# Optimization experiments

Measured on AMD Instinct MI355X. Metric: run time of the kernel, lower is better.

## Reference

```python
import jax, jax.numpy as jnp
import numpy as np

N_NODES = 50000
N_EDGES = 800000


def _glorot(key, shape):
    fan_in, fan_out = shape
    lim = float(np.sqrt(6.0 / (fan_in + fan_out)))
    return jax.random.uniform(key, shape, jnp.float32, -lim, lim)


def setup_inputs() -> dict:
    key = jax.random.key(0)
    ks = jax.random.split(key, 8)
    x = jax.random.normal(ks[0], (N_NODES, 2), jnp.float32)
    edge_index = jax.random.randint(ks[1], (2, N_EDGES), 0, N_NODES, jnp.int64)
    edge_weight = jax.random.uniform(ks[2], (N_EDGES,), jnp.float32)
    return {
        "x": x,
        "edge_index": edge_index,
        "edge_weight": edge_weight,
        "W1": _glorot(ks[3], (2, 128)),
        "b1": jnp.zeros((128,), jnp.float32),
        "W2": _glorot(ks[4], (128, 64)),
        "b2": jnp.zeros((64,), jnp.float32),
        "W3": _glorot(ks[5], (64, 1)),
        "b3": jnp.zeros((1,), jnp.float32),
    }


def _gcn_conv(x, W, b, src, dst, ew, n_nodes):
    # PyG GCNConv with normalize=False: out[i] = sum_{e:(j->i)} ew[e] * (x_j @ W) + b
    h = x @ W                       # [N, F_out] tiny GEMM
    msg = h[src] * ew[:, None]      # [E, F_out] gather + scale
    out = jax.ops.segment_sum(msg, dst, num_segments=n_nodes)  # scatter-add
    return out + b


def reference(x, edge_index, edge_weight, W1, b1, W2, b2, W3, b3):
    src, dst = edge_index[0], edge_index[1]  # source_to_target flow: aggregate at dst
    n = x.shape[0]
    h1 = jax.nn.relu(_gcn_conv(x, W1, b1, src, dst, edge_weight, n))
    # dropout is a no-op in eval mode
    h2 = jax.nn.relu(_gcn_conv(h1, W2, b2, src, dst, edge_weight, n))
    h3 = _gcn_conv(h2, W3, b3, src, dst, edge_weight, n)  # [N, 1]
    return h3.squeeze(-1)  # [N]
```

## Files before the change

### kernel.cpp

```cpp
#include <hip/hip_runtime.h>
#include <hip/hip_fp16.h>

#define N_NODES 50000
#define N_EDGES 800000
#define BSHIFT 7
#define NBKT 391
#define CAP 3072
#define TILE 2048
#define BIN_THREADS 512
#define SL_THREADS 512

typedef _Float16 f16x8 __attribute__((ext_vector_type(8)));
typedef float f32x4 __attribute__((ext_vector_type(4)));
typedef float f32x2 __attribute__((ext_vector_type(2)));

__device__ __forceinline__ float edge_w(unsigned p) {
    return __half2float(__ushort_as_half((unsigned short)(p >> 16)));
}

__device__ __forceinline__ unsigned char f32_to_fp8(float v) {
    int w = __builtin_amdgcn_cvt_pk_fp8_f32(v, v, 0, false);
    return (unsigned char)(w & 0xFF);
}

__global__ __launch_bounds__(BIN_THREADS) void bin_edges(
    const int* __restrict__ src, const int* __restrict__ dstA,
    const float* __restrict__ ew, int* __restrict__ bcur,
    uint2* __restrict__ brec) {
    __shared__ unsigned pk[TILE];
    __shared__ unsigned short sdst[TILE];
    __shared__ uint2 rec[TILE];
    __shared__ int cnt[NBKT];
    __shared__ int lofs[NBKT];
    __shared__ int cbase[NBKT];
    __shared__ int wsum[8];
    __shared__ int wpre[8];

    int t = threadIdx.x;
    int lane = t & 63, wid = t >> 6;
    int e0 = blockIdx.x * TILE;
    int nmax = N_EDGES - e0;
    if (nmax > TILE) nmax = TILE;
    if (nmax < 0) nmax = 0;
    if (t < NBKT) cnt[t] = 0;
    __syncthreads();
    for (int i = t; i < nmax; i += BIN_THREADS) {
        int e = e0 + i;
        int d = dstA[e];
        unsigned hw = (unsigned)__half_as_ushort(__float2half(ew[e]));
        pk[i] = (unsigned)src[e] | (hw << 16);
        sdst[i] = (unsigned short)d;
        atomicAdd(&cnt[d >> BSHIFT], 1);
    }
    __syncthreads();
    int v = (t < NBKT) ? cnt[t] : 0;
    int s = v;
#pragma unroll
    for (int off = 1; off < 64; off <<= 1) {
        int u = __shfl_up(s, off);
        if (lane >= off) s += u;
    }
    if (lane == 63) wsum[wid] = s;
    __syncthreads();
    if (t < 8) {
        int a = 0;
        for (int i = 0; i < t; i++) a += wsum[i];
        wpre[t] = a;
    }
    __syncthreads();
    int incl = s + wpre[wid];
    if (t < NBKT) {
        lofs[t] = incl - v;
        cbase[t] = t * CAP + (v ? atomicAdd(&bcur[t], v) : 0);
        cnt[t] = 0;
    }
    __syncthreads();
    for (int i = t; i < nmax; i += BIN_THREADS) {
        int d = sdst[i];
        int bk = d >> BSHIFT;
        int pos = lofs[bk] + atomicAdd(&cnt[bk], 1);
        rec[pos] = make_uint2(pk[i], (unsigned)d);
    }
    __syncthreads();
    for (int i = t; i < nmax; i += BIN_THREADS) {
        uint2 r = rec[i];
        int bk = (int)(r.y >> BSHIFT);
        int g = cbase[bk] + (i - lofs[bk]);
        brec[g] = r;
    }
}

__global__ __launch_bounds__(SL_THREADS) void sort_l1(
    const int* __restrict__ bcur, const uint2* __restrict__ brec,
    const float* __restrict__ x,
    const float* __restrict__ W1, const float* __restrict__ b1,
    const float* __restrict__ W2,
    unsigned* __restrict__ sorted, int2* __restrict__ rowspan,
    unsigned char* __restrict__ t2) {
    __shared__ unsigned spk[CAP];
    __shared__ int nh[128], lcur[128];
    __shared__ float nodeA[128], nodeB[128];
    __shared__ __align__(16) __half w2t[64][136];
    __shared__ __align__(16) float w1r0[128];
    __shared__ __align__(16) float w1r1[128];
    __shared__ __align__(16) float b1s[128];
    __shared__ int wsum2[2];

    int b = blockIdx.x;
    int t = threadIdx.x;
    int lane = t & 63, wid = t >> 6;
    int base = b * CAP;
    int n = bcur[b];
    if (n > CAP) n = CAP;

    for (int idx = t; idx < 128 * 64; idx += SL_THREADS) {
        int k = idx >> 6, nn = idx & 63;
        w2t[nn][k] = __float2half(W2[idx]);
    }
    if (t < 128) {
        w1r0[t] = W1[t];
        w1r1[t] = W1[128 + t];
        b1s[t]  = b1[t];
        nh[t] = 0;
        lcur[t] = 0;
        nodeA[t] = 0.f;
        nodeB[t] = 0.f;
    }
    __syncthreads();

    unsigned rp[6];
    int rd[6];
#pragma unroll
    for (int i = 0; i < 6; i++) {
        int e = t + i * SL_THREADS;
        if (e < n) {
            uint2 r = brec[base + e];
            rp[i] = r.x;
            rd[i] = (int)(r.y & 127u);
            atomicAdd(&nh[rd[i]], 1);
            float w = edge_w(r.x);
            float2 xv = ((const float2*)x)[r.x & 0xFFFF];
            atomicAdd(&nodeA[rd[i]], w * xv.x);
            atomicAdd(&nodeB[rd[i]], w * xv.y);
        }
    }
    __syncthreads();

    int v = (t < 128) ? nh[t] : 0;
    int s = v;
#pragma unroll
    for (int off = 1; off < 64; off <<= 1) {
        int u = __shfl_up(s, off);
        if (lane >= off) s += u;
    }
    if (lane == 63 && wid < 2) wsum2[wid] = s;
    __syncthreads();
    if (t < 128) {
        int incl = s + (wid ? wsum2[0] : 0);
        int ex = incl - v;
        int node = (b << BSHIFT) + t;
        if (node < N_NODES) rowspan[node] = make_int2(base + ex, base + ex + v);
        nh[t] = ex;
    }
    __syncthreads();

#pragma unroll
    for (int i = 0; i < 6; i++) {
        int e = t + i * SL_THREADS;
        if (e < n) {
            int pos = nh[rd[i]] + atomicAdd(&lcur[rd[i]], 1);
            spk[pos] = rp[i];
        }
    }
    __syncthreads();
    for (int e = t; e < n; e += SL_THREADS) sorted[base + e] = spk[e];

    int wave = t >> 6;
    int m0 = wave * 16;
    int fr = lane & 15;
    int kb = (lane >> 4) * 8;
    float a0 = nodeA[m0 + fr];
    float a1 = nodeB[m0 + fr];
    f32x4 acc0 = {0.f, 0.f, 0.f, 0.f};
    f32x4 acc1 = {0.f, 0.f, 0.f, 0.f};
    f32x4 acc2 = {0.f, 0.f, 0.f, 0.f};
    f32x4 acc3 = {0.f, 0.f, 0.f, 0.f};
#pragma unroll
    for (int k0 = 0; k0 < 128; k0 += 32) {
        f16x8 av;
#pragma unroll
        for (int j = 0; j < 8; j++) {
            int k = k0 + kb + j;
            float h = fmaxf(fmaf(a0, w1r0[k], fmaf(a1, w1r1[k], b1s[k])), 0.f);
            av[j] = (_Float16)h;
        }
        f16x8 bv0 = *(const f16x8*)&w2t[ 0 + fr][k0 + kb];
        f16x8 bv1 = *(const f16x8*)&w2t[16 + fr][k0 + kb];
        f16x8 bv2 = *(const f16x8*)&w2t[32 + fr][k0 + kb];
        f16x8 bv3 = *(const f16x8*)&w2t[48 + fr][k0 + kb];
        acc0 = __builtin_amdgcn_mfma_f32_16x16x32_f16(av, bv0, acc0, 0, 0, 0);
        acc1 = __builtin_amdgcn_mfma_f32_16x16x32_f16(av, bv1, acc1, 0, 0, 0);
        acc2 = __builtin_amdgcn_mfma_f32_16x16x32_f16(av, bv2, acc2, 0, 0, 0);
        acc3 = __builtin_amdgcn_mfma_f32_16x16x32_f16(av, bv3, acc3, 0, 0, 0);
    }
    int rowb = (b << BSHIFT) + m0 + ((lane >> 4) & 3) * 4;
#pragma unroll
    for (int r = 0; r < 4; r++) {
        int node = rowb + r;
        if (node < N_NODES) {
            unsigned char* o = t2 + node * 64 + fr;
            o[0]  = f32_to_fp8(acc0[r]);
            o[16] = f32_to_fp8(acc1[r]);
            o[32] = f32_to_fp8(acc2[r]);
            o[48] = f32_to_fp8(acc3[r]);
        }
    }
}

__global__ void gather2_dot3(const int2* __restrict__ rowspan, const unsigned* __restrict__ sorted,
                             const unsigned char* __restrict__ t2, const float* __restrict__ b2,
                             const float* __restrict__ W3, float* __restrict__ t3) {
    int gtid = blockIdx.x * blockDim.x + threadIdx.x;
    int node = gtid >> 6;
    int lane = threadIdx.x & 63;
    if (node >= N_NODES) return;
    int eg  = lane >> 3;
    int fli = lane & 7;
    int2 sp = rowspan[node];
    float a0 = 0.f, a1 = 0.f, a2 = 0.f, a3 = 0.f, a4 = 0.f, a5 = 0.f, a6 = 0.f, a7 = 0.f;
    int e = sp.x + eg;
    for (; e + 8 < sp.y; e += 16) {
        unsigned p0 = sorted[e];
        unsigned p1 = sorted[e + 8];
        uint2 q0 = *(const uint2*)(t2 + (p0 & 0xFFFF) * 64 + fli * 8);
        uint2 q1 = *(const uint2*)(t2 + (p1 & 0xFFFF) * 64 + fli * 8);
        float w0 = edge_w(p0), w1 = edge_w(p1);
        f32x2 f;
        f = __builtin_amdgcn_cvt_pk_f32_fp8(q0.x, false); a0 = fmaf(w0, f.x, a0); a1 = fmaf(w0, f.y, a1);
        f = __builtin_amdgcn_cvt_pk_f32_fp8(q0.x, true);  a2 = fmaf(w0, f.x, a2); a3 = fmaf(w0, f.y, a3);
        f = __builtin_amdgcn_cvt_pk_f32_fp8(q0.y, false); a4 = fmaf(w0, f.x, a4); a5 = fmaf(w0, f.y, a5);
        f = __builtin_amdgcn_cvt_pk_f32_fp8(q0.y, true);  a6 = fmaf(w0, f.x, a6); a7 = fmaf(w0, f.y, a7);
        f = __builtin_amdgcn_cvt_pk_f32_fp8(q1.x, false); a0 = fmaf(w1, f.x, a0); a1 = fmaf(w1, f.y, a1);
        f = __builtin_amdgcn_cvt_pk_f32_fp8(q1.x, true);  a2 = fmaf(w1, f.x, a2); a3 = fmaf(w1, f.y, a3);
        f = __builtin_amdgcn_cvt_pk_f32_fp8(q1.y, false); a4 = fmaf(w1, f.x, a4); a5 = fmaf(w1, f.y, a5);
        f = __builtin_amdgcn_cvt_pk_f32_fp8(q1.y, true);  a6 = fmaf(w1, f.x, a6); a7 = fmaf(w1, f.y, a7);
    }
    if (e < sp.y) {
        unsigned p = sorted[e];
        uint2 q = *(const uint2*)(t2 + (p & 0xFFFF) * 64 + fli * 8);
        float w = edge_w(p);
        f32x2 f;
        f = __builtin_amdgcn_cvt_pk_f32_fp8(q.x, false); a0 = fmaf(w, f.x, a0); a1 = fmaf(w, f.y, a1);
        f = __builtin_amdgcn_cvt_pk_f32_fp8(q.x, true);  a2 = fmaf(w, f.x, a2); a3 = fmaf(w, f.y, a3);
        f = __builtin_amdgcn_cvt_pk_f32_fp8(q.y, false); a4 = fmaf(w, f.x, a4); a5 = fmaf(w, f.y, a5);
        f = __builtin_amdgcn_cvt_pk_f32_fp8(q.y, true);  a6 = fmaf(w, f.x, a6); a7 = fmaf(w, f.y, a7);
    }
#pragma unroll
    for (int off = 8; off < 64; off <<= 1) {
        a0 += __shfl_xor(a0, off); a1 += __shfl_xor(a1, off);
        a2 += __shfl_xor(a2, off); a3 += __shfl_xor(a3, off);
        a4 += __shfl_xor(a4, off); a5 += __shfl_xor(a5, off);
        a6 += __shfl_xor(a6, off); a7 += __shfl_xor(a7, off);
    }
    float4 bA = *(const float4*)(b2 + fli * 8);
    float4 bB = *(const float4*)(b2 + fli * 8 + 4);
    float4 wA = *(const float4*)(W3 + fli * 8);
    float4 wB = *(const float4*)(W3 + fli * 8 + 4);
    float h = fmaxf(a0 + bA.x, 0.f) * wA.x + fmaxf(a1 + bA.y, 0.f) * wA.y +
              fmaxf(a2 + bA.z, 0.f) * wA.z + fmaxf(a3 + bA.w, 0.f) * wA.w +
              fmaxf(a4 + bB.x, 0.f) * wB.x + fmaxf(a5 + bB.y, 0.f) * wB.y +
              fmaxf(a6 + bB.z, 0.f) * wB.z + fmaxf(a7 + bB.w, 0.f) * wB.w;
#pragma unroll
    for (int off = 1; off < 8; off <<= 1) h += __shfl_xor(h, off);
    if (lane == 0) t3[node] = h;
}

__global__ void gather3(const int2* __restrict__ rowspan, const unsigned* __restrict__ sorted,
                        const float* __restrict__ t3, const float* __restrict__ b3,
                        float* __restrict__ out) {
    int gtid = blockIdx.x * blockDim.x + threadIdx.x;
    int wid = gtid >> 6;
    int lane = threadIdx.x & 63;
    int sub = lane >> 3;
    int sl  = lane & 7;
    int node = wid * 8 + sub;
    if (node >= N_NODES) return;
    int2 sp = rowspan[node];
    float acc = 0.f;
    for (int e = sp.x + sl; e < sp.y; e += 8) {
        unsigned p = sorted[e];
        acc = fmaf(edge_w(p), t3[p & 0xFFFF], acc);
    }
#pragma unroll
    for (int off = 1; off < 8; off <<= 1) acc += __shfl_xor(acc, off);
    if (sl == 0) out[node] = acc + b3[0];
}

extern "C" void kernel_launch(void* const* d_in, const int* in_sizes, int n_in,
                              void* d_out, int out_size, void* d_ws, size_t ws_size,
                              hipStream_t stream) {
    const float* x  = (const float*)d_in[0];
    const int*   ei = (const int*)d_in[1];
    const float* ew = (const float*)d_in[2];
    const float* W1 = (const float*)d_in[3];
    const float* b1 = (const float*)d_in[4];
    const float* W2 = (const float*)d_in[5];
    const float* b2 = (const float*)d_in[6];
    const float* W3 = (const float*)d_in[7];
    const float* b3 = (const float*)d_in[8];
    float* out = (float*)d_out;

    const int* src = ei;
    const int* dst = ei + N_EDGES;

    char* p = (char*)d_ws;
    int*  bcur    = (int*)p;            p += NBKT * sizeof(int);
    p = (char*)(((uintptr_t)p + 15) & ~(uintptr_t)15);
    int2* rowspan = (int2*)p;           p += N_NODES * sizeof(int2);
    uint2* brec   = (uint2*)p;          p += (long)NBKT * CAP * sizeof(uint2);
    unsigned* sorted = (unsigned*)p;    p += (long)NBKT * CAP * sizeof(unsigned);
    unsigned char* t2 = (unsigned char*)p; p += 64L * N_NODES;
    float* t3     = (float*)p;          p += N_NODES * sizeof(float);

    hipMemsetAsync(bcur, 0, NBKT * sizeof(int), stream);

    bin_edges<<<NBKT, BIN_THREADS, 0, stream>>>(src, dst, ew, bcur, brec);

    sort_l1<<<NBKT, SL_THREADS, 0, stream>>>(bcur, brec, x, W1, b1, W2, sorted, rowspan, t2);

    gather2_dot3<<<(N_NODES * 64 + 255) / 256, 256, 0, stream>>>(rowspan, sorted, t2, b2, W3, t3);

    gather3<<<((N_NODES + 7) / 8 * 64 + 255) / 256, 256, 0, stream>>>(rowspan, sorted, t3, b3, out);
}
```

Before: 136.8 us.

## Replace CSR sort and per-node gathers with bucket-local LDS atomic aggregation

Removes the per-bucket counting sort, rowspan and sorted-edge arrays. Layers 2 and 3 now stream the unsorted bucket records and accumulate into shared-memory per-node accumulators with LDS float atomics. Layer 2 is split across two blocks per bucket, each handling half of the features, and the two partial dot products are combined with global atomics into t3, which is zeroed by an enlarged memset. This drops a sort pass and the sorted-array traffic, in exchange for many LDS atomics (8 per edge-subgroup) and nondeterministic float summation order.

```diff
diff --git a/kernel.cpp b/kernel.cpp
--- a/kernel.cpp
+++ b/kernel.cpp
@@ -8,7 +8,7 @@
 #define CAP 3072
 #define TILE 2048
 #define BIN_THREADS 512
-#define SL_THREADS 512
+#define THREADS 512
 
 typedef _Float16 f16x8 __attribute__((ext_vector_type(8)));
 typedef float f32x4 __attribute__((ext_vector_type(4)));
@@ -90,30 +90,24 @@
     }
 }
 
-__global__ __launch_bounds__(SL_THREADS) void sort_l1(
+__global__ __launch_bounds__(THREADS) void l1_mfma(
     const int* __restrict__ bcur, const uint2* __restrict__ brec,
     const float* __restrict__ x,
     const float* __restrict__ W1, const float* __restrict__ b1,
-    const float* __restrict__ W2,
-    unsigned* __restrict__ sorted, int2* __restrict__ rowspan,
-    unsigned char* __restrict__ t2) {
-    __shared__ unsigned spk[CAP];
-    __shared__ int nh[128], lcur[128];
-    __shared__ float nodeA[128], nodeB[128];
+    const float* __restrict__ W2, unsigned char* __restrict__ t2) {
     __shared__ __align__(16) __half w2t[64][136];
     __shared__ __align__(16) float w1r0[128];
     __shared__ __align__(16) float w1r1[128];
     __shared__ __align__(16) float b1s[128];
-    __shared__ int wsum2[2];
+    __shared__ float nodeA[128], nodeB[128];
 
     int b = blockIdx.x;
     int t = threadIdx.x;
-    int lane = t & 63, wid = t >> 6;
     int base = b * CAP;
     int n = bcur[b];
     if (n > CAP) n = CAP;
 
-    for (int idx = t; idx < 128 * 64; idx += SL_THREADS) {
+    for (int idx = t; idx < 128 * 64; idx += THREADS) {
         int k = idx >> 6, nn = idx & 63;
         w2t[nn][k] = __float2half(W2[idx]);
     }
@@ -121,61 +115,22 @@
         w1r0[t] = W1[t];
         w1r1[t] = W1[128 + t];
         b1s[t]  = b1[t];
-        nh[t] = 0;
-        lcur[t] = 0;
         nodeA[t] = 0.f;
         nodeB[t] = 0.f;
     }
     __syncthreads();
 
-    unsigned rp[6];
-    int rd[6];
-#pragma unroll
-    for (int i = 0; i < 6; i++) {
-        int e = t + i * SL_THREADS;
-        if (e < n) {
-            uint2 r = brec[base + e];
-            rp[i] = r.x;
-            rd[i] = (int)(r.y & 127u);
-            atomicAdd(&nh[rd[i]], 1);
-            float w = edge_w(r.x);
-            float2 xv = ((const float2*)x)[r.x & 0xFFFF];
-            atomicAdd(&nodeA[rd[i]], w * xv.x);
-            atomicAdd(&nodeB[rd[i]], w * xv.y);
-        }
-    }
-    __syncthreads();
-
-    int v = (t < 128) ? nh[t] : 0;
-    int s = v;
-#pragma unroll
-    for (int off = 1; off < 64; off <<= 1) {
-        int u = __shfl_up(s, off);
-        if (lane >= off) s += u;
-    }
-    if (lane == 63 && wid < 2) wsum2[wid] = s;
-    __syncthreads();
-    if (t < 128) {
-        int incl = s + (wid ? wsum2[0] : 0);
-        int ex = incl - v;
-        int node = (b << BSHIFT) + t;
-        if (node < N_NODES) rowspan[node] = make_int2(base + ex, base + ex + v);
-        nh[t] = ex;
-    }
-    __syncthreads();
-
-#pragma unroll
-    for (int i = 0; i < 6; i++) {
-        int e = t + i * SL_THREADS;
-        if (e < n) {
-            int pos = nh[rd[i]] + atomicAdd(&lcur[rd[i]], 1);
-            spk[pos] = rp[i];
-        }
-    }
-    __syncthreads();
-    for (int e = t; e < n; e += SL_THREADS) sorted[base + e] = spk[e];
-
-    int wave = t >> 6;
+    for (int e = t; e < n; e += THREADS) {
+        uint2 r = brec[base + e];
+        float w = edge_w(r.x);
+        float2 xv = ((const float2*)x)[r.x & 0xFFFF];
+        int dlow = (int)(r.y & 127u);
+        atomicAdd(&nodeA[dlow], w * xv.x);
+        atomicAdd(&nodeB[dlow], w * xv.y);
+    }
+    __syncthreads();
+
+    int wave = t >> 6, lane = t & 63;
     int m0 = wave * 16;
     int fr = lane & 15;
     int kb = (lane >> 4) * 8;
@@ -203,7 +158,7 @@
         acc2 = __builtin_amdgcn_mfma_f32_16x16x32_f16(av, bv2, acc2, 0, 0, 0);
         acc3 = __builtin_amdgcn_mfma_f32_16x16x32_f16(av, bv3, acc3, 0, 0, 0);
     }
-    int rowb = (b << BSHIFT) + m0 + ((lane >> 4) & 3) * 4;
+    int rowb = (b << BSHIFT) + m0 + (lane >> 4) * 4;
 #pragma unroll
     for (int r = 0; r < 4; r++) {
         int node = rowb + r;
@@ -217,83 +172,75 @@
     }
 }
 
-__global__ void gather2_dot3(const int2* __restrict__ rowspan, const unsigned* __restrict__ sorted,
-                             const unsigned char* __restrict__ t2, const float* __restrict__ b2,
-                             const float* __restrict__ W3, float* __restrict__ t3) {
-    int gtid = blockIdx.x * blockDim.x + threadIdx.x;
-    int node = gtid >> 6;
-    int lane = threadIdx.x & 63;
-    if (node >= N_NODES) return;
-    int eg  = lane >> 3;
-    int fli = lane & 7;
-    int2 sp = rowspan[node];
-    float a0 = 0.f, a1 = 0.f, a2 = 0.f, a3 = 0.f, a4 = 0.f, a5 = 0.f, a6 = 0.f, a7 = 0.f;
-    int e = sp.x + eg;
-    for (; e + 8 < sp.y; e += 16) {
-        unsigned p0 = sorted[e];
-        unsigned p1 = sorted[e + 8];
-        uint2 q0 = *(const uint2*)(t2 + (p0 & 0xFFFF) * 64 + fli * 8);
-        uint2 q1 = *(const uint2*)(t2 + (p1 & 0xFFFF) * 64 + fli * 8);
-        float w0 = edge_w(p0), w1 = edge_w(p1);
+__global__ __launch_bounds__(THREADS) void l2_dot(
+    const int* __restrict__ bcur, const uint2* __restrict__ brec,
+    const unsigned char* __restrict__ t2, const float* __restrict__ b2,
+    const float* __restrict__ W3, float* __restrict__ t3) {
+    __shared__ float hacc[128][36];
+    __shared__ float b2s[32], w3s[32];
+    int bb = blockIdx.x;
+    int b = bb >> 1, half = bb & 1;
+    int t = threadIdx.x;
+    int base = b * CAP;
+    int n = bcur[b];
+    if (n > CAP) n = CAP;
+
+    for (int i = t; i < 128 * 36; i += THREADS) ((float*)hacc)[i] = 0.f;
+    if (t < 32) { b2s[t] = b2[half * 32 + t]; w3s[t] = W3[half * 32 + t]; }
+    __syncthreads();
+
+    int total = n * 4;
+    for (int s = t; s < total; s += THREADS) {
+        int e = s >> 2, sub = s & 3;
+        uint2 r = brec[base + e];
+        float w = edge_w(r.x);
+        int dlow = (int)(r.y & 127u);
+        uint2 q = *(const uint2*)(t2 + (r.x & 0xFFFF) * 64 + half * 32 + sub * 8);
+        float* hrow = &hacc[dlow][sub * 8];
         f32x2 f;
-        f = __builtin_amdgcn_cvt_pk_f32_fp8(q0.x, false); a0 = fmaf(w0, f.x, a0); a1 = fmaf(w0, f.y, a1);
-        f = __builtin_amdgcn_cvt_pk_f32_fp8(q0.x, true);  a2 = fmaf(w0, f.x, a2); a3 = fmaf(w0, f.y, a3);
-        f = __builtin_amdgcn_cvt_pk_f32_fp8(q0.y, false); a4 = fmaf(w0, f.x, a4); a5 = fmaf(w0, f.y, a5);
-        f = __builtin_amdgcn_cvt_pk_f32_fp8(q0.y, true);  a6 = fmaf(w0, f.x, a6); a7 = fmaf(w0, f.y, a7);
-        f = __builtin_amdgcn_cvt_pk_f32_fp8(q1.x, false); a0 = fmaf(w1, f.x, a0); a1 = fmaf(w1, f.y, a1);
-        f = __builtin_amdgcn_cvt_pk_f32_fp8(q1.x, true);  a2 = fmaf(w1, f.x, a2); a3 = fmaf(w1, f.y, a3);
-        f = __builtin_amdgcn_cvt_pk_f32_fp8(q1.y, false); a4 = fmaf(w1, f.x, a4); a5 = fmaf(w1, f.y, a5);
-        f = __builtin_amdgcn_cvt_pk_f32_fp8(q1.y, true);  a6 = fmaf(w1, f.x, a6); a7 = fmaf(w1, f.y, a7);
-    }
-    if (e < sp.y) {
-        unsigned p = sorted[e];
-        uint2 q = *(const uint2*)(t2 + (p & 0xFFFF) * 64 + fli * 8);
-        float w = edge_w(p);
-        f32x2 f;
-        f = __builtin_amdgcn_cvt_pk_f32_fp8(q.x, false); a0 = fmaf(w, f.x, a0); a1 = fmaf(w, f.y, a1);
-        f = __builtin_amdgcn_cvt_pk_f32_fp8(q.x, true);  a2 = fmaf(w, f.x, a2); a3 = fmaf(w, f.y, a3);
-        f = __builtin_amdgcn_cvt_pk_f32_fp8(q.y, false); a4 = fmaf(w, f.x, a4); a5 = fmaf(w, f.y, a5);
-        f = __builtin_amdgcn_cvt_pk_f32_fp8(q.y, true);  a6 = fmaf(w, f.x, a6); a7 = fmaf(w, f.y, a7);
-    }
-#pragma unroll
-    for (int off = 8; off < 64; off <<= 1) {
-        a0 += __shfl_xor(a0, off); a1 += __shfl_xor(a1, off);
-        a2 += __shfl_xor(a2, off); a3 += __shfl_xor(a3, off);
-        a4 += __shfl_xor(a4, off); a5 += __shfl_xor(a5, off);
-        a6 += __shfl_xor(a6, off); a7 += __shfl_xor(a7, off);
-    }
-    float4 bA = *(const float4*)(b2 + fli * 8);
-    float4 bB = *(const float4*)(b2 + fli * 8 + 4);
-    float4 wA = *(const float4*)(W3 + fli * 8);
-    float4 wB = *(const float4*)(W3 + fli * 8 + 4);
-    float h = fmaxf(a0 + bA.x, 0.f) * wA.x + fmaxf(a1 + bA.y, 0.f) * wA.y +
-              fmaxf(a2 + bA.z, 0.f) * wA.z + fmaxf(a3 + bA.w, 0.f) * wA.w +
-              fmaxf(a4 + bB.x, 0.f) * wB.x + fmaxf(a5 + bB.y, 0.f) * wB.y +
-              fmaxf(a6 + bB.z, 0.f) * wB.z + fmaxf(a7 + bB.w, 0.f) * wB.w;
-#pragma unroll
-    for (int off = 1; off < 8; off <<= 1) h += __shfl_xor(h, off);
-    if (lane == 0) t3[node] = h;
-}
-
-__global__ void gather3(const int2* __restrict__ rowspan, const unsigned* __restrict__ sorted,
-                        const float* __restrict__ t3, const float* __restrict__ b3,
-                        float* __restrict__ out) {
-    int gtid = blockIdx.x * blockDim.x + threadIdx.x;
-    int wid = gtid >> 6;
-    int lane = threadIdx.x & 63;
-    int sub = lane >> 3;
-    int sl  = lane & 7;
-    int node = wid * 8 + sub;
-    if (node >= N_NODES) return;
-    int2 sp = rowspan[node];
+        f = __builtin_amdgcn_cvt_pk_f32_fp8(q.x, false);
+        atomicAdd(&hrow[0], w * f.x); atomicAdd(&hrow[1], w * f.y);
+        f = __builtin_amdgcn_cvt_pk_f32_fp8(q.x, true);
+        atomicAdd(&hrow[2], w * f.x); atomicAdd(&hrow[3], w * f.y);
+        f = __builtin_amdgcn_cvt_pk_f32_fp8(q.y, false);
+        atomicAdd(&hrow[4], w * f.x); atomicAdd(&hrow[5], w * f.y);
+        f = __builtin_amdgcn_cvt_pk_f32_fp8(q.y, true);
+        atomicAdd(&hrow[6], w * f.x); atomicAdd(&hrow[7], w * f.y);
+    }
+    __syncthreads();
+
+    int nodeL = t >> 2, q4 = t & 3;
     float acc = 0.f;
-    for (int e = sp.x + sl; e < sp.y; e += 8) {
-        unsigned p = sorted[e];
-        acc = fmaf(edge_w(p), t3[p & 0xFFFF], acc);
-    }
-#pragma unroll
-    for (int off = 1; off < 8; off <<= 1) acc += __shfl_xor(acc, off);
-    if (sl == 0) out[node] = acc + b3[0];
+#pragma unroll
+    for (int j = 0; j < 8; j++) {
+        int d = q4 * 8 + j;
+        acc += fmaxf(hacc[nodeL][d] + b2s[d], 0.f) * w3s[d];
+    }
+    acc += __shfl_xor(acc, 1);
+    acc += __shfl_xor(acc, 2);
+    int node = (b << BSHIFT) + nodeL;
+    if (q4 == 0 && node < N_NODES) atomicAdd(&t3[node], acc);
+}
+
+__global__ __launch_bounds__(THREADS) void l3_out(
+    const int* __restrict__ bcur, const uint2* __restrict__ brec,
+    const float* __restrict__ t3, const float* __restrict__ b3,
+    float* __restrict__ out) {
+    __shared__ float nacc[128];
+    int b = blockIdx.x;
+    int t = threadIdx.x;
+    int base = b * CAP;
+    int n = bcur[b];
+    if (n > CAP) n = CAP;
+    if (t < 128) nacc[t] = 0.f;
+    __syncthreads();
+    for (int e = t; e < n; e += THREADS) {
+        uint2 r = brec[base + e];
+        atomicAdd(&nacc[r.y & 127u], edge_w(r.x) * t3[r.x & 0xFFFF]);
+    }
+    __syncthreads();
+    int node = (b << BSHIFT) + t;
+    if (t < 128 && node < N_NODES) out[node] = nacc[t] + b3[0];
 }
 
 extern "C" void kernel_launch(void* const* d_in, const int* in_sizes, int n_in,
@@ -314,21 +261,21 @@
     const int* dst = ei + N_EDGES;
 
     char* p = (char*)d_ws;
-    int*  bcur    = (int*)p;            p += NBKT * sizeof(int);
+    int*  bcur = (int*)p;               p += NBKT * sizeof(int);
     p = (char*)(((uintptr_t)p + 15) & ~(uintptr_t)15);
-    int2* rowspan = (int2*)p;           p += N_NODES * sizeof(int2);
-    uint2* brec   = (uint2*)p;          p += (long)NBKT * CAP * sizeof(uint2);
-    unsigned* sorted = (unsigned*)p;    p += (long)NBKT * CAP * sizeof(unsigned);
+    float* t3  = (float*)p;             p += N_NODES * sizeof(float);
+    size_t zbytes = (size_t)(p - (char*)d_ws);
+    p = (char*)(((uintptr_t)p + 15) & ~(uintptr_t)15);
+    uint2* brec = (uint2*)p;            p += (long)NBKT * CAP * sizeof(uint2);
     unsigned char* t2 = (unsigned char*)p; p += 64L * N_NODES;
-    float* t3     = (float*)p;          p += N_NODES * sizeof(float);
-
-    hipMemsetAsync(bcur, 0, NBKT * sizeof(int), stream);
+
+    hipMemsetAsync(d_ws, 0, zbytes, stream);
 
     bin_edges<<<NBKT, BIN_THREADS, 0, stream>>>(src, dst, ew, bcur, brec);
 
-    sort_l1<<<NBKT, SL_THREADS, 0, stream>>>(bcur, brec, x, W1, b1, W2, sorted, rowspan, t2);
-
-    gather2_dot3<<<(N_NODES * 64 + 255) / 256, 256, 0, stream>>>(rowspan, sorted, t2, b2, W3, t3);
-
-    gather3<<<((N_NODES + 7) / 8 * 64 + 255) / 256, 256, 0, stream>>>(rowspan, sorted, t3, b3, out);
-}
+    l1_mfma<<<NBKT, THREADS, 0, stream>>>(bcur, brec, x, W1, b1, W2, t2);
+
+    l2_dot<<<NBKT * 2, THREADS, 0, stream>>>(bcur, brec, t2, b2, W3, t3);
+
+    l3_out<<<NBKT, THREADS, 0, stream>>>(bcur, brec, t3, b3, out);
+}
```

New measurement: 453.7 us. 3.32x slower.
